# Optimization experiments

Hardware: AMD Instinct MI355X
Metric: run time of the kernel (lower is better)

The kernel has to match this reference:

```python
import jax, jax.numpy as jnp
import numpy as np

B, L, D, K = 32, 4096, 1024, 64


def setup_inputs() -> dict:
    key = jax.random.key(0)
    k1, k2, k3, k4, k5 = jax.random.split(key, 5)
    feats = jax.random.normal(k1, (B, L, D), dtype=jnp.float32)
    assign_w = jax.random.normal(k2, (K, D), dtype=jnp.float32) * (1.0 / np.sqrt(D))
    assign_b = jax.random.normal(k3, (K,), dtype=jnp.float32) * 0.01
    centroids = jax.random.uniform(k4, (K, D), dtype=jnp.float32)
    # ensure at least one valid token per batch row (softmax over L stays finite)
    lens = jax.random.randint(k5, (B,), L // 2, L + 1, dtype=jnp.int32)
    return {"feats": feats, "lens": lens, "assign_w": assign_w,
            "assign_b": assign_b, "centroids": centroids}


def reference(feats, lens, assign_w, assign_b, centroids):
    # feats: (B,L,D); lens: (B,) int; assign_w: (K,D); assign_b: (K,); centroids: (K,D)
    Bq, Lq, Dq = feats.shape
    # padding mask; torch code slices to max(lens) first, but masked positions
    # contribute zero weight after softmax, so keeping full L is equivalent.
    mask = jnp.arange(Lq)[None, :] < lens[:, None]            # (B,L)
    logits = jnp.einsum('bld,kd->blk', feats, assign_w) + assign_b  # (B,L,K)
    logits = jnp.where(mask[:, :, None], logits, -jnp.inf)
    a = jax.nn.softmax(logits, axis=1)                         # softmax over L
    # (a[:,:,:,None] * (feats[:,:,None,:] - centroids)).sum(1) without
    # materializing the (B,L,K,D) residual tensor:
    s = a.sum(axis=1)                                          # (B,K), == 1 analytically
    vlad = jnp.einsum('blk,bld->bkd', a, feats) - s[..., None] * centroids[None]  # (B,K,D)
    out = vlad.min(axis=1)                                     # min over clusters -> (B,D)
    norm = jnp.maximum(jnp.linalg.norm(out, axis=-1, keepdims=True), 1e-12)
    return out / norm
```

## Files before the change

### kernel.cpp

```cpp
#include <hip/hip_runtime.h>
#include <math.h>

#define NB 32
#define NL 4096
#define ND 1024
#define NK 64
#define DTILE 128
#define S_SPLIT 4

typedef __bf16 bf16_t;
typedef __bf16 bf16x8 __attribute__((ext_vector_type(8)));
typedef __bf16 bf16x4 __attribute__((ext_vector_type(4)));
typedef float f32x4_t __attribute__((ext_vector_type(4)));

__global__ __launch_bounds__(256) void k_convw(const float* __restrict__ W,
                                               bf16_t* __restrict__ Wb) {
    const int i = (blockIdx.x * 256 + threadIdx.x) * 4;
    const float4 v = *(const float4*)(W + i);
    bf16x4 o;
    o[0] = (bf16_t)v.x; o[1] = (bf16_t)v.y; o[2] = (bf16_t)v.z; o[3] = (bf16_t)v.w;
    *(bf16x4*)(Wb + i) = o;
}

__global__ __launch_bounds__(256) void k_logits(const float* __restrict__ feats,
                                                const bf16_t* __restrict__ Wb,
                                                const float* __restrict__ bias,
                                                const int* __restrict__ lens,
                                                float* __restrict__ logitsT,
                                                float* __restrict__ pmax,
                                                float* __restrict__ psum) {
    const int bid = blockIdx.x;
    const int b = bid >> 5;
    const int chunk = bid & 31;
    const int l0 = chunk << 7;
    const int len = lens[b];
    if (l0 >= len) return;
    const int t = threadIdx.x;
    const int w = t >> 6;
    const int lane = t & 63;
    const int lr = lane & 15;
    const int oct = lane >> 4;
    const float* fp0 = feats + ((size_t)b * NL + l0 + w * 32 + lr) * ND + oct * 8;
    const float* fp1 = fp0 + (size_t)16 * ND;

    f32x4_t acc[2][4];
#pragma unroll
    for (int m = 0; m < 2; ++m)
#pragma unroll
        for (int j = 0; j < 4; ++j) acc[m][j] = (f32x4_t){0.f, 0.f, 0.f, 0.f};

#pragma unroll 2
    for (int kk = 0; kk < 32; ++kk) {
        const int d = kk * 32;
        const float4 a0 = *(const float4*)(fp0 + d);
        const float4 a1 = *(const float4*)(fp0 + d + 4);
        const float4 a2 = *(const float4*)(fp1 + d);
        const float4 a3 = *(const float4*)(fp1 + d + 4);
        bf16x8 af0, af1;
        af0[0] = (bf16_t)a0.x; af0[1] = (bf16_t)a0.y; af0[2] = (bf16_t)a0.z; af0[3] = (bf16_t)a0.w;
        af0[4] = (bf16_t)a1.x; af0[5] = (bf16_t)a1.y; af0[6] = (bf16_t)a1.z; af0[7] = (bf16_t)a1.w;
        af1[0] = (bf16_t)a2.x; af1[1] = (bf16_t)a2.y; af1[2] = (bf16_t)a2.z; af1[3] = (bf16_t)a2.w;
        af1[4] = (bf16_t)a3.x; af1[5] = (bf16_t)a3.y; af1[6] = (bf16_t)a3.z; af1[7] = (bf16_t)a3.w;
#pragma unroll
        for (int j = 0; j < 4; ++j) {
            const bf16x8 bf = *(const bf16x8*)(Wb + (size_t)(j * 16 + lr) * ND + d + oct * 8);
            acc[0][j] = __builtin_amdgcn_mfma_f32_16x16x32_bf16(af0, bf, acc[0][j], 0, 0, 0);
            acc[1][j] = __builtin_amdgcn_mfma_f32_16x16x32_bf16(af1, bf, acc[1][j], 0, 0, 0);
        }
    }
    float vals[2][4][4];
#pragma unroll
    for (int m = 0; m < 2; ++m)
#pragma unroll
        for (int j = 0; j < 4; ++j) {
            const int k = j * 16 + lr;
            const float bs = bias[k];
#pragma unroll
            for (int r = 0; r < 4; ++r) vals[m][j][r] = acc[m][j][r] + bs;
            const int lb = l0 + w * 32 + m * 16 + oct * 4;
            float4 st = make_float4(vals[m][j][0], vals[m][j][1], vals[m][j][2], vals[m][j][3]);
            *(float4*)(logitsT + ((size_t)b * NK + k) * NL + lb) = st;
        }
    __shared__ float red[64][33];
    __shared__ float bm[64];
    const int slot = w * 8 + oct * 2;
#pragma unroll
    for (int m = 0; m < 2; ++m) {
        const int lbase = l0 + w * 32 + m * 16 + oct * 4;
#pragma unroll
        for (int j = 0; j < 4; ++j) {
            float vm = -1e30f;
#pragma unroll
            for (int r = 0; r < 4; ++r)
                if (lbase + r < len) vm = fmaxf(vm, vals[m][j][r]);
            red[j * 16 + lr][slot + m] = vm;
        }
    }
    __syncthreads();
    if (t < 64) {
        float m = -1e30f;
#pragma unroll
        for (int q = 0; q < 32; ++q) m = fmaxf(m, red[t][q]);
        bm[t] = m;
    }
    __syncthreads();
#pragma unroll
    for (int m = 0; m < 2; ++m) {
        const int lbase = l0 + w * 32 + m * 16 + oct * 4;
#pragma unroll
        for (int j = 0; j < 4; ++j) {
            const float mk = bm[j * 16 + lr];
            float sj = 0.f;
#pragma unroll
            for (int r = 0; r < 4; ++r)
                if (lbase + r < len) sj += __expf(vals[m][j][r] - mk);
            red[j * 16 + lr][slot + m] = sj;
        }
    }
    __syncthreads();
    if (t < 64) {
        float ssum = 0.f;
#pragma unroll
        for (int q = 0; q < 32; ++q) ssum += red[t][q];
        pmax[((size_t)b * 32 + chunk) * 64 + t] = bm[t];
        psum[((size_t)b * 32 + chunk) * 64 + t] = ssum;
    }
}

__global__ void k_sm2(const float* __restrict__ pmax, const float* __restrict__ psum,
                      const int* __restrict__ lens,
                      float* __restrict__ mbuf2) {
    const int b = blockIdx.x;
    const int k = threadIdx.x;
    const int nc = (lens[b] + 127) >> 7;
    float m = -1e30f;
    for (int c = 0; c < nc; ++c) m = fmaxf(m, pmax[((size_t)b * 32 + c) * 64 + k]);
    float s = 0.f;
    for (int c = 0; c < nc; ++c)
        s += psum[((size_t)b * 32 + c) * 64 + k] * __expf(pmax[((size_t)b * 32 + c) * 64 + k] - m);
    mbuf2[b * 64 + k] = m + logf(s);
}

__global__ __launch_bounds__(256, 4) void k_aggregate(const float* __restrict__ feats,
                                                      const float* __restrict__ logitsT,
                                                      const int* __restrict__ lens,
                                                      const float* __restrict__ mbuf2,
                                                      float* __restrict__ pO) {
    const int bid = blockIdx.x;
    const int s  = bid & 3;
    const int dc = (bid >> 2) & 7;
    const int b  = bid >> 5;
    const int d0 = dc * DTILE;
    const int t = threadIdx.x;
    const int w = t >> 6;
    const int lane = t & 63;
    const int lr = lane & 15;
    const int oct = lane >> 4;
    const int len = lens[b];
    const int nT = (len + 63) >> 6;
    const int t0 = (nT * s) >> 2;
    const int t1 = (nT * (s + 1)) >> 2;

    __shared__ char fH[16 * 1024];

    const int kk = w * 16 + lr;
    const float ms2k = mbuf2[b * 64 + kk];
    const float* lgrow = logitsT + ((size_t)b * NK + kk) * NL;

    const int c4 = (t & 31) * 4;
    const int lf0 = (t >> 5) * 4;

    f32x4_t acc[8];
#pragma unroll
    for (int n = 0; n < 8; ++n) acc[n] = (f32x4_t){0.f, 0.f, 0.f, 0.f};

    float4 plg[4];
    float4 pf[2][4];

#define LOADT(tile_)                                                                     \
    {                                                                                    \
        const int lb_ = (tile_) * 64;                                                    \
        plg[0] = *(const float4*)(lgrow + lb_ + oct * 8);                                \
        plg[1] = *(const float4*)(lgrow + lb_ + oct * 8 + 4);                            \
        plg[2] = *(const float4*)(lgrow + lb_ + 32 + oct * 8);                           \
        plg[3] = *(const float4*)(lgrow + lb_ + 32 + oct * 8 + 4);                       \
        _Pragma("unroll")                                                                \
        for (int p_ = 0; p_ < 2; ++p_) {                                                 \
            _Pragma("unroll")                                                            \
            for (int i_ = 0; i_ < 4; ++i_)                                               \
                pf[p_][i_] = *(const float4*)(feats +                                    \
                    ((size_t)b * NL + lb_ + p_ * 32 + lf0 + i_) * ND + d0 + c4);         \
        }                                                                                \
    }

    if (t0 < t1) LOADT(t0);

    for (int tile = t0; tile < t1; ++tile) {
        const int l0 = tile * 64;
        bf16x8 afH[2], afL[2];
#pragma unroll
        for (int ks = 0; ks < 2; ++ks) {
#pragma unroll
            for (int h = 0; h < 2; ++h) {
                const float4 v = plg[ks * 2 + h];
                const int lbase = l0 + ks * 32 + oct * 8 + h * 4;
                float av[4];
                av[0] = (lbase + 0 < len) ? __expf(v.x - ms2k) : 0.f;
                av[1] = (lbase + 1 < len) ? __expf(v.y - ms2k) : 0.f;
                av[2] = (lbase + 2 < len) ? __expf(v.z - ms2k) : 0.f;
                av[3] = (lbase + 3 < len) ? __expf(v.w - ms2k) : 0.f;
#pragma unroll
                for (int c = 0; c < 4; ++c) {
                    const bf16_t hi = (bf16_t)av[c];
                    afH[ks][h * 4 + c] = hi;
                    afL[ks][h * 4 + c] = (bf16_t)(av[c] - (float)hi);
                }
            }
        }
        __syncthreads();
#pragma unroll
        for (int p = 0; p < 2; ++p) {
            const int l4 = p * 32 + lf0;
#pragma unroll
            for (int j = 0; j < 4; ++j) {
                const int d = c4 + j;
                bf16x4 hi;
                hi[0] = (bf16_t)(&pf[p][0].x)[j];
                hi[1] = (bf16_t)(&pf[p][1].x)[j];
                hi[2] = (bf16_t)(&pf[p][2].x)[j];
                hi[3] = (bf16_t)(&pf[p][3].x)[j];
                const int chunk = (l4 >> 3) ^ ((d ^ (d >> 3)) & 7);
                const int off = d * 128 + (chunk << 4) + (l4 & 7) * 2;
                *(bf16x4*)(fH + off) = hi;
            }
        }
        if (tile + 1 < t1) LOADT(tile + 1);
        __syncthreads();
#pragma unroll
        for (int ks = 0; ks < 2; ++ks) {
            const int cbase = ks * 4 + oct;
#pragma unroll
            for (int n = 0; n < 8; ++n) {
                const int d = n * 16 + lr;
                const int foff = d * 128 + ((cbase ^ ((d ^ (d >> 3)) & 7)) << 4);
                const bf16x8 bfH = *(const bf16x8*)(fH + foff);
                acc[n] = __builtin_amdgcn_mfma_f32_16x16x32_bf16(afH[ks], bfH, acc[n], 0, 0, 0);
                acc[n] = __builtin_amdgcn_mfma_f32_16x16x32_bf16(afL[ks], bfH, acc[n], 0, 0, 0);
            }
        }
    }
#undef LOADT
    float* po = pO + ((size_t)((b * 8 + dc) * S_SPLIT + s)) * (NK * DTILE);
#pragma unroll
    for (int n = 0; n < 8; ++n) {
#pragma unroll
        for (int r = 0; r < 4; ++r) {
            const int k = w * 16 + oct * 4 + r;
            po[k * DTILE + n * 16 + lr] = acc[n][r];
        }
    }
}

__global__ __launch_bounds__(128) void k_combine(const float* __restrict__ pO,
                                                 const float* __restrict__ centroids,
                                                 float* __restrict__ outun) {
    const int b = blockIdx.x >> 3;
    const int d = (blockIdx.x & 7) * 128 + threadIdx.x;
    const int dc = d >> 7;
    const int dl = d & 127;
    const float* base = pO + ((size_t)(b * 8 + dc)) * S_SPLIT * NK * DTILE;
    float mn = 1e30f;
    for (int k = 0; k < NK; ++k) {
        float v = 0.f;
#pragma unroll
        for (int s = 0; s < S_SPLIT; ++s) v += base[(size_t)(s * NK + k) * DTILE + dl];
        v -= centroids[(size_t)k * ND + d];
        mn = fminf(mn, v);
    }
    outun[(size_t)b * ND + d] = mn;
}

__global__ __launch_bounds__(256) void k_norm(const float* __restrict__ outun,
                                              float* __restrict__ out) {
    const int b = blockIdx.x;
    const int t = threadIdx.x;
    float ss = 0.f;
    for (int d = t; d < ND; d += 256) {
        const float v = outun[(size_t)b * ND + d];
        ss += v * v;
    }
#pragma unroll
    for (int off = 32; off > 0; off >>= 1) ss += __shfl_down(ss, off);
    __shared__ float red[4];
    if ((t & 63) == 0) red[t >> 6] = ss;
    __syncthreads();
    const float tot = red[0] + red[1] + red[2] + red[3];
    const float inv = 1.0f / fmaxf(sqrtf(tot), 1e-12f);
    for (int d = t; d < ND; d += 256) out[(size_t)b * ND + d] = outun[(size_t)b * ND + d] * inv;
}

extern "C" void kernel_launch(void* const* d_in, const int* in_sizes, int n_in,
                              void* d_out, int out_size, void* d_ws, size_t ws_size,
                              hipStream_t stream) {
    const float* feats     = (const float*)d_in[0];
    const int*   lens      = (const int*)d_in[1];
    const float* W         = (const float*)d_in[2];
    const float* bias      = (const float*)d_in[3];
    const float* centroids = (const float*)d_in[4];
    float* out = (float*)d_out;

    char* ws = (char*)d_ws;
    size_t off = 0;
    bf16_t* Wb     = (bf16_t*)(ws + off); off += (size_t)NK * ND * sizeof(bf16_t);
    float* logitsT = (float*)(ws + off);  off += (size_t)NB * NL * NK * sizeof(float);
    float* pmax    = (float*)(ws + off);  off += (size_t)NB * 32 * NK * sizeof(float);
    float* psum    = (float*)(ws + off);  off += (size_t)NB * 32 * NK * sizeof(float);
    float* mbuf2   = (float*)(ws + off);  off += (size_t)NB * NK * sizeof(float);
    float* outun   = (float*)(ws + off);  off += (size_t)NB * ND * sizeof(float);
    float* pO      = (float*)(ws + off);

    k_convw<<<NK * ND / 1024, 256, 0, stream>>>(W, Wb);
    k_logits<<<NB * (NL / 128), 256, 0, stream>>>(feats, Wb, bias, lens, logitsT, pmax, psum);
    k_sm2<<<NB, 64, 0, stream>>>(pmax, psum, lens, mbuf2);
    k_aggregate<<<NB * 8 * S_SPLIT, 256, 0, stream>>>(feats, logitsT, lens, mbuf2, pO);
    k_combine<<<NB * 8, 128, 0, stream>>>(pO, centroids, outun);
    k_norm<<<NB, 256, 0, stream>>>(outun, out);
}
```

Before: 284.6 us.

## Fuse logits, online softmax and aggregation into one split-L kernel

Replaces the separate logits, softmax-stats and aggregation kernels with one fused kernel. Each 512-thread block handles one L-slice of a batch across the full D, computes the logits for each 64-row tile in-register, keeps a running per-cluster max and sum, and rescales its MFMA accumulators flash-attention style. This removes the logitsT write/read and the dedicated stats kernel, and reuses each feats tile from LDS and cache rather than re-reading it in a later kernel. In exchange, the per-split partial outputs grow to a full K×D per block, which adds a large write in the fused kernel and a large read in combine. The LDS footprint of about 150 KB per block limits each CU to one block, and a small gstats kernel is added to merge the softmax statistics.

```diff
diff --git a/kernel.cpp b/kernel.cpp
--- a/kernel.cpp
+++ b/kernel.cpp
@@ -5,13 +5,17 @@
 #define NL 4096
 #define ND 1024
 #define NK 64
-#define DTILE 128
-#define S_SPLIT 4
+#define NSPLIT 16
 
 typedef __bf16 bf16_t;
 typedef __bf16 bf16x8 __attribute__((ext_vector_type(8)));
 typedef __bf16 bf16x4 __attribute__((ext_vector_type(4)));
 typedef float f32x4_t __attribute__((ext_vector_type(4)));
+
+__device__ __forceinline__ unsigned short bfbits(float x) {
+    bf16_t h = (bf16_t)x;
+    return __builtin_bit_cast(unsigned short, h);
+}
 
 __global__ __launch_bounds__(256) void k_convw(const float* __restrict__ W,
                                                bf16_t* __restrict__ Wb) {
@@ -22,135 +26,16 @@
     *(bf16x4*)(Wb + i) = o;
 }
 
-__global__ __launch_bounds__(256) void k_logits(const float* __restrict__ feats,
-                                                const bf16_t* __restrict__ Wb,
-                                                const float* __restrict__ bias,
-                                                const int* __restrict__ lens,
-                                                float* __restrict__ logitsT,
-                                                float* __restrict__ pmax,
-                                                float* __restrict__ psum) {
+__global__ __launch_bounds__(512, 2) void k_fused(const float* __restrict__ feats,
+                                                  const bf16_t* __restrict__ Wb,
+                                                  const float* __restrict__ bias,
+                                                  const int* __restrict__ lens,
+                                                  float* __restrict__ pO,
+                                                  float* __restrict__ mS,
+                                                  float* __restrict__ sS) {
     const int bid = blockIdx.x;
-    const int b = bid >> 5;
-    const int chunk = bid & 31;
-    const int l0 = chunk << 7;
-    const int len = lens[b];
-    if (l0 >= len) return;
-    const int t = threadIdx.x;
-    const int w = t >> 6;
-    const int lane = t & 63;
-    const int lr = lane & 15;
-    const int oct = lane >> 4;
-    const float* fp0 = feats + ((size_t)b * NL + l0 + w * 32 + lr) * ND + oct * 8;
-    const float* fp1 = fp0 + (size_t)16 * ND;
-
-    f32x4_t acc[2][4];
-#pragma unroll
-    for (int m = 0; m < 2; ++m)
-#pragma unroll
-        for (int j = 0; j < 4; ++j) acc[m][j] = (f32x4_t){0.f, 0.f, 0.f, 0.f};
-
-#pragma unroll 2
-    for (int kk = 0; kk < 32; ++kk) {
-        const int d = kk * 32;
-        const float4 a0 = *(const float4*)(fp0 + d);
-        const float4 a1 = *(const float4*)(fp0 + d + 4);
-        const float4 a2 = *(const float4*)(fp1 + d);
-        const float4 a3 = *(const float4*)(fp1 + d + 4);
-        bf16x8 af0, af1;
-        af0[0] = (bf16_t)a0.x; af0[1] = (bf16_t)a0.y; af0[2] = (bf16_t)a0.z; af0[3] = (bf16_t)a0.w;
-        af0[4] = (bf16_t)a1.x; af0[5] = (bf16_t)a1.y; af0[6] = (bf16_t)a1.z; af0[7] = (bf16_t)a1.w;
-        af1[0] = (bf16_t)a2.x; af1[1] = (bf16_t)a2.y; af1[2] = (bf16_t)a2.z; af1[3] = (bf16_t)a2.w;
-        af1[4] = (bf16_t)a3.x; af1[5] = (bf16_t)a3.y; af1[6] = (bf16_t)a3.z; af1[7] = (bf16_t)a3.w;
-#pragma unroll
-        for (int j = 0; j < 4; ++j) {
-            const bf16x8 bf = *(const bf16x8*)(Wb + (size_t)(j * 16 + lr) * ND + d + oct * 8);
-            acc[0][j] = __builtin_amdgcn_mfma_f32_16x16x32_bf16(af0, bf, acc[0][j], 0, 0, 0);
-            acc[1][j] = __builtin_amdgcn_mfma_f32_16x16x32_bf16(af1, bf, acc[1][j], 0, 0, 0);
-        }
-    }
-    float vals[2][4][4];
-#pragma unroll
-    for (int m = 0; m < 2; ++m)
-#pragma unroll
-        for (int j = 0; j < 4; ++j) {
-            const int k = j * 16 + lr;
-            const float bs = bias[k];
-#pragma unroll
-            for (int r = 0; r < 4; ++r) vals[m][j][r] = acc[m][j][r] + bs;
-            const int lb = l0 + w * 32 + m * 16 + oct * 4;
-            float4 st = make_float4(vals[m][j][0], vals[m][j][1], vals[m][j][2], vals[m][j][3]);
-            *(float4*)(logitsT + ((size_t)b * NK + k) * NL + lb) = st;
-        }
-    __shared__ float red[64][33];
-    __shared__ float bm[64];
-    const int slot = w * 8 + oct * 2;
-#pragma unroll
-    for (int m = 0; m < 2; ++m) {
-        const int lbase = l0 + w * 32 + m * 16 + oct * 4;
-#pragma unroll
-        for (int j = 0; j < 4; ++j) {
-            float vm = -1e30f;
-#pragma unroll
-            for (int r = 0; r < 4; ++r)
-                if (lbase + r < len) vm = fmaxf(vm, vals[m][j][r]);
-            red[j * 16 + lr][slot + m] = vm;
-        }
-    }
-    __syncthreads();
-    if (t < 64) {
-        float m = -1e30f;
-#pragma unroll
-        for (int q = 0; q < 32; ++q) m = fmaxf(m, red[t][q]);
-        bm[t] = m;
-    }
-    __syncthreads();
-#pragma unroll
-    for (int m = 0; m < 2; ++m) {
-        const int lbase = l0 + w * 32 + m * 16 + oct * 4;
-#pragma unroll
-        for (int j = 0; j < 4; ++j) {
-            const float mk = bm[j * 16 + lr];
-            float sj = 0.f;
-#pragma unroll
-            for (int r = 0; r < 4; ++r)
-                if (lbase + r < len) sj += __expf(vals[m][j][r] - mk);
-            red[j * 16 + lr][slot + m] = sj;
-        }
-    }
-    __syncthreads();
-    if (t < 64) {
-        float ssum = 0.f;
-#pragma unroll
-        for (int q = 0; q < 32; ++q) ssum += red[t][q];
-        pmax[((size_t)b * 32 + chunk) * 64 + t] = bm[t];
-        psum[((size_t)b * 32 + chunk) * 64 + t] = ssum;
-    }
-}
-
-__global__ void k_sm2(const float* __restrict__ pmax, const float* __restrict__ psum,
-                      const int* __restrict__ lens,
-                      float* __restrict__ mbuf2) {
-    const int b = blockIdx.x;
-    const int k = threadIdx.x;
-    const int nc = (lens[b] + 127) >> 7;
-    float m = -1e30f;
-    for (int c = 0; c < nc; ++c) m = fmaxf(m, pmax[((size_t)b * 32 + c) * 64 + k]);
-    float s = 0.f;
-    for (int c = 0; c < nc; ++c)
-        s += psum[((size_t)b * 32 + c) * 64 + k] * __expf(pmax[((size_t)b * 32 + c) * 64 + k] - m);
-    mbuf2[b * 64 + k] = m + logf(s);
-}
-
-__global__ __launch_bounds__(256, 4) void k_aggregate(const float* __restrict__ feats,
-                                                      const float* __restrict__ logitsT,
-                                                      const int* __restrict__ lens,
-                                                      const float* __restrict__ mbuf2,
-                                                      float* __restrict__ pO) {
-    const int bid = blockIdx.x;
-    const int s  = bid & 3;
-    const int dc = (bid >> 2) & 7;
-    const int b  = bid >> 5;
-    const int d0 = dc * DTILE;
+    const int b  = bid >> 4;
+    const int sp = bid & 15;
     const int t = threadIdx.x;
     const int w = t >> 6;
     const int lane = t & 63;
@@ -158,122 +43,256 @@
     const int oct = lane >> 4;
     const int len = lens[b];
     const int nT = (len + 63) >> 6;
-    const int t0 = (nT * s) >> 2;
-    const int t1 = (nT * (s + 1)) >> 2;
-
-    __shared__ char fH[16 * 1024];
-
-    const int kk = w * 16 + lr;
-    const float ms2k = mbuf2[b * 64 + kk];
-    const float* lgrow = logitsT + ((size_t)b * NK + kk) * NL;
-
-    const int c4 = (t & 31) * 4;
-    const int lf0 = (t >> 5) * 4;
-
-    f32x4_t acc[8];
-#pragma unroll
-    for (int n = 0; n < 8; ++n) acc[n] = (f32x4_t){0.f, 0.f, 0.f, 0.f};
-
-    float4 plg[4];
-    float4 pf[2][4];
-
-#define LOADT(tile_)                                                                     \
-    {                                                                                    \
-        const int lb_ = (tile_) * 64;                                                    \
-        plg[0] = *(const float4*)(lgrow + lb_ + oct * 8);                                \
-        plg[1] = *(const float4*)(lgrow + lb_ + oct * 8 + 4);                            \
-        plg[2] = *(const float4*)(lgrow + lb_ + 32 + oct * 8);                           \
-        plg[3] = *(const float4*)(lgrow + lb_ + 32 + oct * 8 + 4);                       \
-        _Pragma("unroll")                                                                \
-        for (int p_ = 0; p_ < 2; ++p_) {                                                 \
-            _Pragma("unroll")                                                            \
-            for (int i_ = 0; i_ < 4; ++i_)                                               \
-                pf[p_][i_] = *(const float4*)(feats +                                    \
-                    ((size_t)b * NL + lb_ + p_ * 32 + lf0 + i_) * ND + d0 + c4);         \
-        }                                                                                \
-    }
-
-    if (t0 < t1) LOADT(t0);
+    const int t0 = (nT * sp) >> 4;
+    const int t1 = (nT * (sp + 1)) >> 4;
+
+    extern __shared__ char lds[];
+    char*  const fT   = lds;
+    char*  const lgT  = lds + 131072;
+    float* const red  = (float*)(lds + 147456);
+    float* const mrun = (float*)(lds + 151808);
+    float* const srun = (float*)(lds + 152064);
+    float* const mnew = (float*)(lds + 152320);
+    float* const rA   = (float*)(lds + 152576);
+
+    const int mtg = w >> 2, jq = w & 3;
+    const int kh  = w & 1,  dh = w >> 1;
+    const int dgrp = (t & 127) * 8;
+    const int lgq  = t >> 7;
+
+    const int kA = jq * 16 + lr;
+    const float bs = bias[kA];
+    const int kk0 = kh * 32 + lr;
+
+    if (t < 64) { mrun[t] = -1e30f; srun[t] = 0.f; }
+
+    f32x4_t acc[2][16];
+#pragma unroll
+    for (int mi = 0; mi < 2; ++mi)
+#pragma unroll
+        for (int nt = 0; nt < 16; ++nt) acc[mi][nt] = (f32x4_t){0.f, 0.f, 0.f, 0.f};
 
     for (int tile = t0; tile < t1; ++tile) {
         const int l0 = tile * 64;
-        bf16x8 afH[2], afL[2];
+        __syncthreads();
+
+#pragma unroll
+        for (int half = 0; half < 2; ++half) {
+            const int lbase = lgq * 16 + half * 8;
+            unsigned cu[8][4];
+#pragma unroll
+            for (int lw = 0; lw < 4; ++lw) {
+                const float* r0 = feats + ((size_t)b * NL + l0 + lbase + lw * 2) * ND + dgrp;
+                const float* r1 = r0 + ND;
+                const float4 a0 = *(const float4*)r0;
+                const float4 a1 = *(const float4*)(r0 + 4);
+                const float4 b0 = *(const float4*)r1;
+                const float4 b1 = *(const float4*)(r1 + 4);
+                cu[0][lw] = bfbits(a0.x) | ((unsigned)bfbits(b0.x) << 16);
+                cu[1][lw] = bfbits(a0.y) | ((unsigned)bfbits(b0.y) << 16);
+                cu[2][lw] = bfbits(a0.z) | ((unsigned)bfbits(b0.z) << 16);
+                cu[3][lw] = bfbits(a0.w) | ((unsigned)bfbits(b0.w) << 16);
+                cu[4][lw] = bfbits(a1.x) | ((unsigned)bfbits(b1.x) << 16);
+                cu[5][lw] = bfbits(a1.y) | ((unsigned)bfbits(b1.y) << 16);
+                cu[6][lw] = bfbits(a1.z) | ((unsigned)bfbits(b1.z) << 16);
+                cu[7][lw] = bfbits(a1.w) | ((unsigned)bfbits(b1.w) << 16);
+            }
+#pragma unroll
+            for (int j = 0; j < 8; ++j) {
+                const int d = dgrp + j;
+                const int c = (lbase >> 3) ^ ((d ^ (d >> 3)) & 7);
+                *(uint4*)(fT + d * 128 + c * 16) =
+                    make_uint4(cu[j][0], cu[j][1], cu[j][2], cu[j][3]);
+            }
+        }
+
+        float vals[2][4];
+        {
+            const float* fp0 = feats + ((size_t)b * NL + l0 + (mtg * 2 + 0) * 16 + lr) * ND + oct * 8;
+            const float* fp1 = feats + ((size_t)b * NL + l0 + (mtg * 2 + 1) * 16 + lr) * ND + oct * 8;
+            const bf16_t* wr = Wb + (size_t)kA * ND + oct * 8;
+            f32x4_t la0 = (f32x4_t){0.f, 0.f, 0.f, 0.f};
+            f32x4_t la1 = (f32x4_t){0.f, 0.f, 0.f, 0.f};
+#pragma unroll 2
+            for (int kk = 0; kk < 32; ++kk) {
+                const int d = kk * 32;
+                const float4 a0 = *(const float4*)(fp0 + d);
+                const float4 a1 = *(const float4*)(fp0 + d + 4);
+                const float4 c0 = *(const float4*)(fp1 + d);
+                const float4 c1 = *(const float4*)(fp1 + d + 4);
+                bf16x8 af0, af1;
+                af0[0] = (bf16_t)a0.x; af0[1] = (bf16_t)a0.y; af0[2] = (bf16_t)a0.z; af0[3] = (bf16_t)a0.w;
+                af0[4] = (bf16_t)a1.x; af0[5] = (bf16_t)a1.y; af0[6] = (bf16_t)a1.z; af0[7] = (bf16_t)a1.w;
+                af1[0] = (bf16_t)c0.x; af1[1] = (bf16_t)c0.y; af1[2] = (bf16_t)c0.z; af1[3] = (bf16_t)c0.w;
+                af1[4] = (bf16_t)c1.x; af1[5] = (bf16_t)c1.y; af1[6] = (bf16_t)c1.z; af1[7] = (bf16_t)c1.w;
+                const bf16x8 bf = *(const bf16x8*)(wr + d);
+                la0 = __builtin_amdgcn_mfma_f32_16x16x32_bf16(af0, bf, la0, 0, 0, 0);
+                la1 = __builtin_amdgcn_mfma_f32_16x16x32_bf16(af1, bf, la1, 0, 0, 0);
+            }
+#pragma unroll
+            for (int r = 0; r < 4; ++r) { vals[0][r] = la0[r] + bs; vals[1][r] = la1[r] + bs; }
+        }
+#pragma unroll
+        for (int mi = 0; mi < 2; ++mi) {
+            const int mt = mtg * 2 + mi;
+            const int c = (mt * 4 + oct) ^ (kA & 15);
+            *(float4*)(lgT + kA * 256 + c * 16) =
+                make_float4(vals[mi][0], vals[mi][1], vals[mi][2], vals[mi][3]);
+            const int lb = l0 + mt * 16 + oct * 4;
+            float vm = -1e30f;
+#pragma unroll
+            for (int r = 0; r < 4; ++r)
+                if (lb + r < len) vm = fmaxf(vm, vals[mi][r]);
+            red[kA * 17 + mt * 4 + oct] = vm;
+        }
+        __syncthreads();
+
+        if (t < 64) {
+            float mc = red[t * 17];
+#pragma unroll
+            for (int q = 1; q < 16; ++q) mc = fmaxf(mc, red[t * 17 + q]);
+            const float mo = mrun[t];
+            const float mn_ = fmaxf(mo, mc);
+            mnew[t] = mn_;
+            rA[t] = __expf(mo - mn_);
+            mrun[t] = mn_;
+        }
+        __syncthreads();
+
+        {
+            const float mk = mnew[kA];
+#pragma unroll
+            for (int mi = 0; mi < 2; ++mi) {
+                const int mt = mtg * 2 + mi;
+                const int lb = l0 + mt * 16 + oct * 4;
+                float sj = 0.f;
+#pragma unroll
+                for (int r = 0; r < 4; ++r)
+                    if (lb + r < len) sj += __expf(vals[mi][r] - mk);
+                red[kA * 17 + mt * 4 + oct] = sj;
+            }
+        }
+        __syncthreads();
+
+        if (t < 64) {
+            float sc_ = 0.f;
+#pragma unroll
+            for (int q = 0; q < 16; ++q) sc_ += red[t * 17 + q];
+            srun[t] = srun[t] * rA[t] + sc_;
+        }
+
+        {
+            const float4 ra0 = *(const float4*)&rA[kh * 32 + oct * 4];
+            const float4 ra1 = *(const float4*)&rA[kh * 32 + 16 + oct * 4];
+#pragma unroll
+            for (int nt = 0; nt < 16; ++nt) {
+                acc[0][nt][0] *= ra0.x; acc[0][nt][1] *= ra0.y;
+                acc[0][nt][2] *= ra0.z; acc[0][nt][3] *= ra0.w;
+                acc[1][nt][0] *= ra1.x; acc[1][nt][1] *= ra1.y;
+                acc[1][nt][2] *= ra1.z; acc[1][nt][3] *= ra1.w;
+            }
+        }
+
+        bf16x8 afH[2][2], afL[2][2];
+#pragma unroll
+        for (int mi = 0; mi < 2; ++mi) {
+            const int kkm = kk0 + mi * 16;
+            const float mk = mnew[kkm];
+#pragma unroll
+            for (int ks = 0; ks < 2; ++ks) {
+                const int c0 = (ks * 8 + oct * 2) ^ lr;
+                const int c1 = (ks * 8 + oct * 2 + 1) ^ lr;
+                const float4 g0 = *(const float4*)(lgT + kkm * 256 + c0 * 16);
+                const float4 g1 = *(const float4*)(lgT + kkm * 256 + c1 * 16);
+                const int lb = l0 + ks * 32 + oct * 8;
+                float e0 = (lb + 0 < len) ? __expf(g0.x - mk) : 0.f;
+                float e1 = (lb + 1 < len) ? __expf(g0.y - mk) : 0.f;
+                float e2 = (lb + 2 < len) ? __expf(g0.z - mk) : 0.f;
+                float e3 = (lb + 3 < len) ? __expf(g0.w - mk) : 0.f;
+                float e4 = (lb + 4 < len) ? __expf(g1.x - mk) : 0.f;
+                float e5 = (lb + 5 < len) ? __expf(g1.y - mk) : 0.f;
+                float e6 = (lb + 6 < len) ? __expf(g1.z - mk) : 0.f;
+                float e7 = (lb + 7 < len) ? __expf(g1.w - mk) : 0.f;
+                bf16x8 h, l2;
+                h[0] = (bf16_t)e0; l2[0] = (bf16_t)(e0 - (float)h[0]);
+                h[1] = (bf16_t)e1; l2[1] = (bf16_t)(e1 - (float)h[1]);
+                h[2] = (bf16_t)e2; l2[2] = (bf16_t)(e2 - (float)h[2]);
+                h[3] = (bf16_t)e3; l2[3] = (bf16_t)(e3 - (float)h[3]);
+                h[4] = (bf16_t)e4; l2[4] = (bf16_t)(e4 - (float)h[4]);
+                h[5] = (bf16_t)e5; l2[5] = (bf16_t)(e5 - (float)h[5]);
+                h[6] = (bf16_t)e6; l2[6] = (bf16_t)(e6 - (float)h[6]);
+                h[7] = (bf16_t)e7; l2[7] = (bf16_t)(e7 - (float)h[7]);
+                afH[mi][ks] = h; afL[mi][ks] = l2;
+            }
+        }
+
 #pragma unroll
         for (int ks = 0; ks < 2; ++ks) {
 #pragma unroll
-            for (int h = 0; h < 2; ++h) {
-                const float4 v = plg[ks * 2 + h];
-                const int lbase = l0 + ks * 32 + oct * 8 + h * 4;
-                float av[4];
-                av[0] = (lbase + 0 < len) ? __expf(v.x - ms2k) : 0.f;
-                av[1] = (lbase + 1 < len) ? __expf(v.y - ms2k) : 0.f;
-                av[2] = (lbase + 2 < len) ? __expf(v.z - ms2k) : 0.f;
-                av[3] = (lbase + 3 < len) ? __expf(v.w - ms2k) : 0.f;
-#pragma unroll
-                for (int c = 0; c < 4; ++c) {
-                    const bf16_t hi = (bf16_t)av[c];
-                    afH[ks][h * 4 + c] = hi;
-                    afL[ks][h * 4 + c] = (bf16_t)(av[c] - (float)hi);
-                }
-            }
-        }
-        __syncthreads();
-#pragma unroll
-        for (int p = 0; p < 2; ++p) {
-            const int l4 = p * 32 + lf0;
-#pragma unroll
-            for (int j = 0; j < 4; ++j) {
-                const int d = c4 + j;
-                bf16x4 hi;
-                hi[0] = (bf16_t)(&pf[p][0].x)[j];
-                hi[1] = (bf16_t)(&pf[p][1].x)[j];
-                hi[2] = (bf16_t)(&pf[p][2].x)[j];
-                hi[3] = (bf16_t)(&pf[p][3].x)[j];
-                const int chunk = (l4 >> 3) ^ ((d ^ (d >> 3)) & 7);
-                const int off = d * 128 + (chunk << 4) + (l4 & 7) * 2;
-                *(bf16x4*)(fH + off) = hi;
-            }
-        }
-        if (tile + 1 < t1) LOADT(tile + 1);
-        __syncthreads();
-#pragma unroll
-        for (int ks = 0; ks < 2; ++ks) {
-            const int cbase = ks * 4 + oct;
-#pragma unroll
-            for (int n = 0; n < 8; ++n) {
-                const int d = n * 16 + lr;
-                const int foff = d * 128 + ((cbase ^ ((d ^ (d >> 3)) & 7)) << 4);
-                const bf16x8 bfH = *(const bf16x8*)(fH + foff);
-                acc[n] = __builtin_amdgcn_mfma_f32_16x16x32_bf16(afH[ks], bfH, acc[n], 0, 0, 0);
-                acc[n] = __builtin_amdgcn_mfma_f32_16x16x32_bf16(afL[ks], bfH, acc[n], 0, 0, 0);
+            for (int nt = 0; nt < 16; ++nt) {
+                const int d = dh * 256 + nt * 16 + lr;
+                const int c = (ks * 4 + oct) ^ ((d ^ (d >> 3)) & 7);
+                const bf16x8 bv = *(const bf16x8*)(fT + d * 128 + c * 16);
+                acc[0][nt] = __builtin_amdgcn_mfma_f32_16x16x32_bf16(afH[0][ks], bv, acc[0][nt], 0, 0, 0);
+                acc[0][nt] = __builtin_amdgcn_mfma_f32_16x16x32_bf16(afL[0][ks], bv, acc[0][nt], 0, 0, 0);
+                acc[1][nt] = __builtin_amdgcn_mfma_f32_16x16x32_bf16(afH[1][ks], bv, acc[1][nt], 0, 0, 0);
+                acc[1][nt] = __builtin_amdgcn_mfma_f32_16x16x32_bf16(afL[1][ks], bv, acc[1][nt], 0, 0, 0);
             }
         }
     }
-#undef LOADT
-    float* po = pO + ((size_t)((b * 8 + dc) * S_SPLIT + s)) * (NK * DTILE);
-#pragma unroll
-    for (int n = 0; n < 8; ++n) {
-#pragma unroll
-        for (int r = 0; r < 4; ++r) {
-            const int k = w * 16 + oct * 4 + r;
-            po[k * DTILE + n * 16 + lr] = acc[n][r];
-        }
+
+    float* po = pO + (size_t)(b * NSPLIT + sp) * NK * ND;
+#pragma unroll
+    for (int mi = 0; mi < 2; ++mi)
+#pragma unroll
+        for (int nt = 0; nt < 16; ++nt) {
+            const int d = dh * 256 + nt * 16 + lr;
+#pragma unroll
+            for (int r = 0; r < 4; ++r) {
+                const int k = kh * 32 + mi * 16 + oct * 4 + r;
+                po[(size_t)k * ND + d] = acc[mi][nt][r];
+            }
+        }
+    if (t < 64) {
+        mS[(size_t)(b * NSPLIT + sp) * 64 + t] = mrun[t];
+        sS[(size_t)(b * NSPLIT + sp) * 64 + t] = srun[t];
     }
 }
 
+__global__ void k_gstats(const float* __restrict__ mS, const float* __restrict__ sS,
+                         float* __restrict__ scale) {
+    const int b = blockIdx.x;
+    const int k = threadIdx.x;
+    float M = -1e30f;
+#pragma unroll
+    for (int s = 0; s < NSPLIT; ++s) M = fmaxf(M, mS[(b * NSPLIT + s) * 64 + k]);
+    float S = 0.f;
+#pragma unroll
+    for (int s = 0; s < NSPLIT; ++s)
+        S += sS[(b * NSPLIT + s) * 64 + k] * __expf(mS[(b * NSPLIT + s) * 64 + k] - M);
+    const float inv = 1.f / S;
+#pragma unroll
+    for (int s = 0; s < NSPLIT; ++s)
+        scale[(b * NSPLIT + s) * 64 + k] = __expf(mS[(b * NSPLIT + s) * 64 + k] - M) * inv;
+}
+
 __global__ __launch_bounds__(128) void k_combine(const float* __restrict__ pO,
+                                                 const float* __restrict__ scale,
                                                  const float* __restrict__ centroids,
                                                  float* __restrict__ outun) {
     const int b = blockIdx.x >> 3;
     const int d = (blockIdx.x & 7) * 128 + threadIdx.x;
-    const int dc = d >> 7;
-    const int dl = d & 127;
-    const float* base = pO + ((size_t)(b * 8 + dc)) * S_SPLIT * NK * DTILE;
+    __shared__ float sc[NSPLIT][64];
+    for (int i = threadIdx.x; i < NSPLIT * 64; i += 128)
+        sc[i >> 6][i & 63] = scale[b * NSPLIT * 64 + i];
+    __syncthreads();
+    const float* pb = pO + (size_t)b * NSPLIT * NK * ND;
     float mn = 1e30f;
     for (int k = 0; k < NK; ++k) {
         float v = 0.f;
 #pragma unroll
-        for (int s = 0; s < S_SPLIT; ++s) v += base[(size_t)(s * NK + k) * DTILE + dl];
+        for (int s = 0; s < NSPLIT; ++s)
+            v += pb[(size_t)(s * NK + k) * ND + d] * sc[s][k];
         v -= centroids[(size_t)k * ND + d];
         mn = fminf(mn, v);
     }
@@ -311,18 +330,18 @@
 
     char* ws = (char*)d_ws;
     size_t off = 0;
-    bf16_t* Wb     = (bf16_t*)(ws + off); off += (size_t)NK * ND * sizeof(bf16_t);
-    float* logitsT = (float*)(ws + off);  off += (size_t)NB * NL * NK * sizeof(float);
-    float* pmax    = (float*)(ws + off);  off += (size_t)NB * 32 * NK * sizeof(float);
-    float* psum    = (float*)(ws + off);  off += (size_t)NB * 32 * NK * sizeof(float);
-    float* mbuf2   = (float*)(ws + off);  off += (size_t)NB * NK * sizeof(float);
-    float* outun   = (float*)(ws + off);  off += (size_t)NB * ND * sizeof(float);
-    float* pO      = (float*)(ws + off);
+    bf16_t* Wb   = (bf16_t*)(ws + off); off += (size_t)NK * ND * sizeof(bf16_t);
+    float* pO    = (float*)(ws + off);  off += (size_t)NB * NSPLIT * NK * ND * sizeof(float);
+    float* mS    = (float*)(ws + off);  off += (size_t)NB * NSPLIT * 64 * sizeof(float);
+    float* sS    = (float*)(ws + off);  off += (size_t)NB * NSPLIT * 64 * sizeof(float);
+    float* scale = (float*)(ws + off);  off += (size_t)NB * NSPLIT * 64 * sizeof(float);
+    float* outun = (float*)(ws + off);  off += (size_t)NB * ND * sizeof(float);
+
+    const size_t LDSB = 152832;
 
     k_convw<<<NK * ND / 1024, 256, 0, stream>>>(W, Wb);
-    k_logits<<<NB * (NL / 128), 256, 0, stream>>>(feats, Wb, bias, lens, logitsT, pmax, psum);
-    k_sm2<<<NB, 64, 0, stream>>>(pmax, psum, lens, mbuf2);
-    k_aggregate<<<NB * 8 * S_SPLIT, 256, 0, stream>>>(feats, logitsT, lens, mbuf2, pO);
-    k_combine<<<NB * 8, 128, 0, stream>>>(pO, centroids, outun);
+    k_fused<<<NB * NSPLIT, 512, LDSB, stream>>>(feats, Wb, bias, lens, pO, mS, sS);
+    k_gstats<<<NB, 64, 0, stream>>>(mS, sS, scale);
+    k_combine<<<NB * 8, 128, 0, stream>>>(pO, scale, centroids, outun);
     k_norm<<<NB, 256, 0, stream>>>(outun, out);
 }
```

After: 534.3 us. +87.8%, slower.
